# Performance work log

Hardware: AMD Instinct MI355X
Metric: run time of the kernel (lower is better)

The kernel has to match this reference:

```python
import jax, jax.numpy as jnp
import numpy as np

G, B, N, D = 3, 4096, 32, 256
C, H, A, L = 128, 8, 128, 16


def setup_inputs() -> dict:
    key = jax.random.key(0)
    ks = jax.random.split(key, 9)
    return {
        "targets": jax.random.normal(ks[0], (B, D), jnp.float32),
        "contexts": jax.random.normal(ks[1], (G, B, N, D), jnp.float32),
        "kernel": jax.random.normal(ks[2], (D, C), jnp.float32) * 0.05,
        "attn_kernel": jax.random.normal(ks[3], (1, H, 2 * C), jnp.float32) * 0.05,
        "attn_bias": jnp.zeros((H * C,), jnp.float32),
        "sem_kernel": jax.random.normal(ks[4], (H * C, A), jnp.float32) * 0.05,
        "sem_att_kernel": jax.random.normal(ks[5], (A, 1), jnp.float32) * 0.05,
        "dense_w": jax.random.normal(ks[6], (H * C, L), jnp.float32) * 0.05,
        "dense_b": jnp.zeros((L,), jnp.float32),
    }


def reference(targets, contexts, kernel, attn_kernel, attn_bias, sem_kernel,
              sem_att_kernel, dense_w, dense_b):
    # NodeAttention (shared weights across metapath groups; vectorized over G)
    node = jnp.einsum('bd,dc->bc', targets, kernel)            # [B,C]
    neigh = jnp.einsum('gbnd,dc->gbnc', contexts, kernel)      # [G,B,N,C]
    g, b, n, c = neigh.shape
    ak = attn_kernel[0]                                        # [H,2C]
    ak_node, ak_neigh = ak[:, :c], ak[:, c:]                   # split of concat([node, neigh])
    # scores[g,b,n,h] = concat(node_b, neigh_gbn) . ak_h
    scores = (jnp.einsum('bc,hc->bh', node, ak_node)[None, :, None, :]
              + jnp.einsum('gbnc,hc->gbnh', neigh, ak_neigh))  # [G,B,N,H]
    scores = jnp.transpose(scores, (0, 1, 3, 2))               # [G,B,H,N]
    coef = jax.nn.softmax(jax.nn.leaky_relu(scores, 0.2), axis=-1)
    z = jnp.einsum('gbhn,gbnc->gbhc', coef, neigh)             # [G,B,H,C]
    z = z.reshape(g, b, -1) + attn_bias                        # [G,B,H*C] (concat=True)
    # SemanticAttention over metapath groups
    inp = jnp.transpose(z, (1, 0, 2))                          # [B,G,HC]
    s = jnp.squeeze(jnp.matmul(jnp.tanh(jnp.matmul(inp, sem_kernel)), sem_att_kernel), -1)  # [B,G]
    att = jax.nn.softmax(s, axis=-1)
    pooled = jnp.einsum('bg,bgd->bd', att, inp)                # [B,HC]
    logits = pooled @ dense_w + dense_b                        # [B,L]
    return logits
```

## Files before the change

kernel.cpp:

```cpp
#include <hip/hip_runtime.h>

typedef float v4f __attribute__((ext_vector_type(4)));
typedef short v8s __attribute__((ext_vector_type(8)));
typedef short v4s __attribute__((ext_vector_type(4)));

__device__ __forceinline__ unsigned short f2bf(float x){
    unsigned u = __float_as_uint(x);
    u += 0x7FFFu + ((u >> 16) & 1u);
    return (unsigned short)(u >> 16);
}
__device__ __forceinline__ float bf2f(unsigned short h){
    return __uint_as_float(((unsigned)h) << 16);
}

__global__ __launch_bounds__(256) void prep_a(const float* __restrict__ kern,
        const float* __restrict__ ak, float* __restrict__ wn, float* __restrict__ wg){
    int d = threadIdx.x;
    float an[8], ag[8];
    #pragma unroll
    for (int h=0;h<8;h++){ an[h]=0.f; ag[h]=0.f; }
    for (int c=0;c<128;c++){
        float kv = kern[d*128+c];
        #pragma unroll
        for (int h=0;h<8;h++){
            an[h] = fmaf(kv, ak[h*256+c], an[h]);
            ag[h] = fmaf(kv, ak[h*256+128+c], ag[h]);
        }
    }
    #pragma unroll
    for (int h=0;h<8;h++){ wn[d*8+h]=an[h]; wg[d*8+h]=ag[h]; }
}

__global__ __launch_bounds__(256) void prep_b(const float* __restrict__ kern,
        const float* __restrict__ wg, unsigned short* __restrict__ packB){
    int tid = blockIdx.x*256 + threadIdx.x;
    for (int r=0;r<9;r++){
        int e = tid + r*4096;
        int j = e & 7; int rest = e >> 3;
        int l = rest & 63; rest >>= 6;
        int cc = rest % 9; int kk = rest / 9;
        int d = kk*32 + (l>>4)*8 + j;
        int c = cc*16 + (l&15);
        float v;
        if (cc < 8) v = kern[d*128 + c];
        else { int h = c - 128; v = (h < 8) ? wg[d*8+h] : 0.0f; }
        packB[e] = f2bf(v);
    }
}

__global__ __launch_bounds__(256) void prep_c(const float* __restrict__ targ,
        const float* __restrict__ wn, float* __restrict__ ns){
    int b = blockIdx.x*256 + threadIdx.x;
    float acc[8];
    #pragma unroll
    for (int h=0;h<8;h++) acc[h]=0.f;
    for (int d=0; d<256; d++){
        float tv = targ[b*256+d];
        #pragma unroll
        for (int h=0;h<8;h++) acc[h] = fmaf(tv, wn[d*8+h], acc[h]);
    }
    #pragma unroll
    for (int h=0;h<8;h++) ns[b*8+h] = acc[h];
}

__global__ __launch_bounds__(256) void prep_d(const float* __restrict__ semk,
        unsigned short* __restrict__ pack2){
    int tid = blockIdx.x*256 + threadIdx.x;
    for (int r=0;r<16;r++){
        int e = tid + r*8192;
        int j = e & 7; int rest = e >> 3;
        int l = rest & 63; rest >>= 6;
        int cc = rest & 7; rest >>= 3;
        int kk = rest & 7; int kc = rest >> 3;
        int k = kc*256 + kk*32 + (l>>4)*8 + j;
        int a = cc*16 + (l&15);
        pack2[e] = f2bf(semk[k*128 + a]);
    }
}

__global__ __launch_bounds__(256) void phase1(const float* __restrict__ ctx,
        const unsigned short* __restrict__ packB, const float* __restrict__ ns,
        const float* __restrict__ bias, unsigned short* __restrict__ zb16){
    __shared__ __align__(16) unsigned short aT[64*256];
    __shared__ __align__(16) unsigned short outT[64*146];
    __shared__ float cf[2*32*8];

    int t = threadIdx.x;
    int bid = blockIdx.x;
    int g  = bid >> 11;
    int b0 = (bid & 2047) * 2;
    const float* cbase = ctx + (size_t)(g*4096 + b0) * 8192;

    int w = t >> 6, lane = t & 63;
    int ncc = (w==0) ? 3 : 2;
    int ccl[3] = {w, w+4, 8};
    v4f acc[4][3];
    #pragma unroll
    for (int m=0;m<4;m++)
        #pragma unroll
        for (int i=0;i<3;i++) acc[m][i] = (v4f){0.f,0.f,0.f,0.f};

    int srow = t >> 5;
    int sd   = (t & 31) * 4;

    v4f pf[8];
    #pragma unroll
    for (int i=0;i<8;i++)
        pf[i] = *(const v4f*)(cbase + (i*8 + srow)*256 + sd);
    #pragma unroll
    for (int i=0;i<8;i++){
        int row = i*8 + srow;
        v4s h;
        h[0]=(short)f2bf(pf[i][0]); h[1]=(short)f2bf(pf[i][1]);
        h[2]=(short)f2bf(pf[i][2]); h[3]=(short)f2bf(pf[i][3]);
        int byte = row*512 + ((sd*2) ^ ((row&7)<<4));
        *(v4s*)((char*)aT + byte) = h;
    }
    __syncthreads();

    #pragma unroll
    for (int i=0;i<8;i++)
        pf[i] = *(const v4f*)(cbase + (i*8 + srow)*256 + 128 + sd);

    #pragma unroll
    for (int kk=0;kk<4;kk++){
        v8s bfr[3];
        #pragma unroll
        for (int i=0;i<3;i++)
            if (i < ncc)
                bfr[i] = *(const v8s*)(packB + (((kk*9 + ccl[i])*64 + lane) << 3));
        v8s afr[4];
        #pragma unroll
        for (int m=0;m<4;m++){
            int row = m*16 + (lane&15);
            int d0  = kk*32 + (lane>>4)*8;
            int byte = row*512 + ((d0*2) ^ ((row&7)<<4));
            afr[m] = *(const v8s*)((const char*)aT + byte);
        }
        #pragma unroll
        for (int m=0;m<4;m++)
            #pragma unroll
            for (int i=0;i<3;i++)
                if (i < ncc)
                    acc[m][i] = __builtin_amdgcn_mfma_f32_16x16x32_bf16(afr[m], bfr[i], acc[m][i], 0,0,0);
    }

    #pragma unroll
    for (int i=0;i<8;i++){
        int row = i*8 + srow;
        int d = 128 + sd;
        v4s h;
        h[0]=(short)f2bf(pf[i][0]); h[1]=(short)f2bf(pf[i][1]);
        h[2]=(short)f2bf(pf[i][2]); h[3]=(short)f2bf(pf[i][3]);
        int byte = row*512 + ((d*2) ^ ((row&7)<<4));
        *(v4s*)((char*)aT + byte) = h;
    }
    __syncthreads();

    #pragma unroll
    for (int kk=4;kk<8;kk++){
        v8s bfr[3];
        #pragma unroll
        for (int i=0;i<3;i++)
            if (i < ncc)
                bfr[i] = *(const v8s*)(packB + (((kk*9 + ccl[i])*64 + lane) << 3));
        v8s afr[4];
        #pragma unroll
        for (int m=0;m<4;m++){
            int row = m*16 + (lane&15);
            int d0  = kk*32 + (lane>>4)*8;
            int byte = row*512 + ((d0*2) ^ ((row&7)<<4));
            afr[m] = *(const v8s*)((const char*)aT + byte);
        }
        #pragma unroll
        for (int m=0;m<4;m++)
            #pragma unroll
            for (int i=0;i<3;i++)
                if (i < ncc)
                    acc[m][i] = __builtin_amdgcn_mfma_f32_16x16x32_bf16(afr[m], bfr[i], acc[m][i], 0,0,0);
    }

    #pragma unroll
    for (int m=0;m<4;m++)
        #pragma unroll
        for (int i=0;i<3;i++)
            if (i < ncc){
                int col = ccl[i]*16 + (lane&15);
                #pragma unroll
                for (int r=0;r<4;r++){
                    int row = m*16 + (lane>>4)*4 + r;
                    outT[row*146 + col] = f2bf(acc[m][i][r]);
                }
            }
    __syncthreads();

    {
        int p = t >> 4, i = t & 15;
        int b = p >> 3, h = p & 7;
        float nsv = ns[(b0 + b)*8 + h];
        int row0 = b*32 + i, row1 = row0 + 16;
        float s0 = bf2f(outT[row0*146 + 128 + h]) + nsv;
        float s1 = bf2f(outT[row1*146 + 128 + h]) + nsv;
        s0 = s0 > 0.f ? s0 : 0.2f*s0;
        s1 = s1 > 0.f ? s1 : 0.2f*s1;
        float m = fmaxf(s0, s1);
        #pragma unroll
        for (int d=1; d<16; d<<=1) m = fmaxf(m, __shfl_xor(m, d));
        float e0 = __expf(s0 - m), e1 = __expf(s1 - m);
        float ssum = e0 + e1;
        #pragma unroll
        for (int d=1; d<16; d<<=1) ssum += __shfl_xor(ssum, d);
        float inv = 1.0f / ssum;
        cf[(b*32 + i)*8 + h]      = e0 * inv;
        cf[(b*32 + i + 16)*8 + h] = e1 * inv;
    }
    __syncthreads();

    {
        int b = t >> 7, c = t & 127;
        float az[8];
        #pragma unroll
        for (int h=0;h<8;h++) az[h]=0.f;
        for (int n=0;n<32;n++){
            float v = bf2f(outT[(b*32+n)*146 + c]);
            v4f c0 = *(const v4f*)&cf[(b*32+n)*8];
            v4f c1 = *(const v4f*)&cf[(b*32+n)*8 + 4];
            az[0] = fmaf(c0[0], v, az[0]); az[1] = fmaf(c0[1], v, az[1]);
            az[2] = fmaf(c0[2], v, az[2]); az[3] = fmaf(c0[3], v, az[3]);
            az[4] = fmaf(c1[0], v, az[4]); az[5] = fmaf(c1[1], v, az[5]);
            az[6] = fmaf(c1[2], v, az[6]); az[7] = fmaf(c1[3], v, az[7]);
        }
        size_t zb = ((size_t)(b0 + b)*3 + g)*1024;
        #pragma unroll
        for (int h=0;h<8;h++) zb16[zb + h*128 + c] = f2bf(az[h] + bias[h*128 + c]);
    }
}

__global__ __launch_bounds__(256) void semk2(const unsigned short* __restrict__ zb16,
        const unsigned short* __restrict__ pack2, const float* __restrict__ sa,
        float* __restrict__ sws){
    __shared__ float red[16*4];
    int t = threadIdx.x, w = t>>6, lane = t&63;
    int r0 = blockIdx.x * 16;
    v4f acc0 = (v4f){0.f,0.f,0.f,0.f};
    v4f acc1 = (v4f){0.f,0.f,0.f,0.f};
    const unsigned short* abase = zb16 + (size_t)(r0 + (lane&15))*1024 + (lane>>4)*8;
    #pragma unroll 4
    for (int kk=0; kk<32; kk++){
        v8s afr = *(const v8s*)(abase + kk*32);
        v8s b0  = *(const v8s*)(pack2 + (((kk*8 + w  )*64 + lane) << 3));
        v8s b1  = *(const v8s*)(pack2 + (((kk*8 + w+4)*64 + lane) << 3));
        acc0 = __builtin_amdgcn_mfma_f32_16x16x32_bf16(afr, b0, acc0, 0,0,0);
        acc1 = __builtin_amdgcn_mfma_f32_16x16x32_bf16(afr, b1, acc1, 0,0,0);
    }
    float sa0 = sa[w*16 + (lane&15)];
    float sa1 = sa[(w+4)*16 + (lane&15)];
    #pragma unroll
    for (int r=0;r<4;r++){
        float v = fmaf(tanhf(acc0[r]), sa0, tanhf(acc1[r]) * sa1);
        #pragma unroll
        for (int d=1; d<16; d<<=1) v += __shfl_xor(v, d);
        if ((lane&15)==0) red[((lane>>4)*4 + r)*4 + w] = v;
    }
    __syncthreads();
    if (t < 16)
        sws[r0 + t] = red[t*4] + red[t*4+1] + red[t*4+2] + red[t*4+3];
}

__global__ __launch_bounds__(64) void final3(const unsigned short* __restrict__ zb16,
        const float* __restrict__ sws, const float* __restrict__ dw,
        const float* __restrict__ db, float* __restrict__ outp){
    int b = blockIdx.x;
    int lane = threadIdx.x;
    float s0 = sws[b*3], s1 = sws[b*3+1], s2 = sws[b*3+2];
    float m = fmaxf(s0, fmaxf(s1, s2));
    float e0 = __expf(s0-m), e1 = __expf(s1-m), e2 = __expf(s2-m);
    float inv = 1.0f/(e0+e1+e2);
    float a0 = e0*inv, a1 = e1*inv, a2 = e2*inv;

    const unsigned short* z0 = zb16 + (size_t)b*3072 + lane*16;
    v8s za0 = *(const v8s*)(z0);          v8s za1 = *(const v8s*)(z0+8);
    v8s zb0 = *(const v8s*)(z0+1024);     v8s zb1 = *(const v8s*)(z0+1032);
    v8s zc0 = *(const v8s*)(z0+2048);     v8s zc1 = *(const v8s*)(z0+2056);
    float p[16];
    #pragma unroll
    for (int k=0;k<8;k++){
        p[k]   = a0*bf2f((unsigned short)za0[k]) + a1*bf2f((unsigned short)zb0[k]) + a2*bf2f((unsigned short)zc0[k]);
        p[k+8] = a0*bf2f((unsigned short)za1[k]) + a1*bf2f((unsigned short)zb1[k]) + a2*bf2f((unsigned short)zc1[k]);
    }
    float acc[16];
    #pragma unroll
    for (int l=0;l<16;l++) acc[l]=0.f;
    #pragma unroll
    for (int k=0;k<16;k++){
        const float* dr = dw + (lane*16 + k)*16;
        v4f d0 = *(const v4f*)(dr);
        v4f d1 = *(const v4f*)(dr+4);
        v4f d2 = *(const v4f*)(dr+8);
        v4f d3 = *(const v4f*)(dr+12);
        float pk = p[k];
        acc[0]=fmaf(pk,d0[0],acc[0]);  acc[1]=fmaf(pk,d0[1],acc[1]);
        acc[2]=fmaf(pk,d0[2],acc[2]);  acc[3]=fmaf(pk,d0[3],acc[3]);
        acc[4]=fmaf(pk,d1[0],acc[4]);  acc[5]=fmaf(pk,d1[1],acc[5]);
        acc[6]=fmaf(pk,d1[2],acc[6]);  acc[7]=fmaf(pk,d1[3],acc[7]);
        acc[8]=fmaf(pk,d2[0],acc[8]);  acc[9]=fmaf(pk,d2[1],acc[9]);
        acc[10]=fmaf(pk,d2[2],acc[10]); acc[11]=fmaf(pk,d2[3],acc[11]);
        acc[12]=fmaf(pk,d3[0],acc[12]); acc[13]=fmaf(pk,d3[1],acc[13]);
        acc[14]=fmaf(pk,d3[2],acc[14]); acc[15]=fmaf(pk,d3[3],acc[15]);
    }
    #pragma unroll
    for (int l=0;l<16;l++){
        float v = acc[l];
        #pragma unroll
        for (int d=1; d<64; d<<=1) v += __shfl_xor(v, d);
        acc[l] = v;
    }
    float myv = 0.f;
    #pragma unroll
    for (int l=0;l<16;l++) myv = (lane==l) ? acc[l] : myv;
    if (lane < 16) outp[b*16 + lane] = myv + db[lane];
}

extern "C" void kernel_launch(void* const* d_in, const int* in_sizes, int n_in,
                              void* d_out, int out_size, void* d_ws, size_t ws_size,
                              hipStream_t stream) {
    const float* targets  = (const float*)d_in[0];
    const float* contexts = (const float*)d_in[1];
    const float* kern     = (const float*)d_in[2];
    const float* ak       = (const float*)d_in[3];
    const float* bias     = (const float*)d_in[4];
    const float* semk     = (const float*)d_in[5];
    const float* sa       = (const float*)d_in[6];
    const float* dw       = (const float*)d_in[7];
    const float* db       = (const float*)d_in[8];
    float* outp = (float*)d_out;

    char* ws = (char*)d_ws;
    unsigned short* packB = (unsigned short*)(ws);
    float* wn             = (float*)(ws + 73728);
    float* wg             = (float*)(ws + 81920);
    float* nsb            = (float*)(ws + 90112);
    unsigned short* pack2 = (unsigned short*)(ws + 221184);
    unsigned short* zb16  = (unsigned short*)(ws + 483328);
    float* sws            = (float*)(ws + 25649152);

    prep_a<<<1, 256, 0, stream>>>(kern, ak, wn, wg);
    prep_b<<<16, 256, 0, stream>>>(kern, wg, packB);
    prep_c<<<16, 256, 0, stream>>>(targets, wn, nsb);
    prep_d<<<32, 256, 0, stream>>>(semk, pack2);
    phase1<<<6144, 256, 0, stream>>>(contexts, packB, nsb, bias, zb16);
    semk2<<<768, 256, 0, stream>>>(zb16, pack2, sa, sws);
    final3<<<4096, 64, 0, stream>>>(zb16, sws, dw, db, outp);
}
```

Baseline: 227.5 us.

## Fuse prep kernels and load context directly into MFMA fragments without LDS staging

The four preprocessing kernels become one prep_all launch, and each block recomputes the small attention-weight projection in shared memory instead of going through a separate kernel and global buffers. In phase1 each wave now loads its own 16 context rows straight from global memory into bf16 MFMA A-fragments and computes all 9 output column tiles. This drops the 32KB LDS staging buffer and two barriers, and launch bounds now ask for 4 blocks per CU. The cost is more B-fragment loads per wave, less coalesced strided global reads, and a larger accumulator register footprint.

```diff
diff --git a/kernel.cpp b/kernel.cpp
--- a/kernel.cpp
+++ b/kernel.cpp
@@ -1,8 +1,8 @@
 #include <hip/hip_runtime.h>
+#include <hip/hip_bf16.h>
 
 typedef float v4f __attribute__((ext_vector_type(4)));
 typedef short v8s __attribute__((ext_vector_type(8)));
-typedef short v4s __attribute__((ext_vector_type(4)));
 
 __device__ __forceinline__ unsigned short f2bf(float x){
     unsigned u = __float_as_uint(x);
@@ -12,76 +12,91 @@
 __device__ __forceinline__ float bf2f(unsigned short h){
     return __uint_as_float(((unsigned)h) << 16);
 }
-
-__global__ __launch_bounds__(256) void prep_a(const float* __restrict__ kern,
-        const float* __restrict__ ak, float* __restrict__ wn, float* __restrict__ wg){
-    int d = threadIdx.x;
-    float an[8], ag[8];
-    #pragma unroll
-    for (int h=0;h<8;h++){ an[h]=0.f; ag[h]=0.f; }
-    for (int c=0;c<128;c++){
-        float kv = kern[d*128+c];
-        #pragma unroll
-        for (int h=0;h<8;h++){
-            an[h] = fmaf(kv, ak[h*256+c], an[h]);
-            ag[h] = fmaf(kv, ak[h*256+128+c], ag[h]);
-        }
-    }
-    #pragma unroll
-    for (int h=0;h<8;h++){ wn[d*8+h]=an[h]; wg[d*8+h]=ag[h]; }
-}
-
-__global__ __launch_bounds__(256) void prep_b(const float* __restrict__ kern,
-        const float* __restrict__ wg, unsigned short* __restrict__ packB){
-    int tid = blockIdx.x*256 + threadIdx.x;
-    for (int r=0;r<9;r++){
-        int e = tid + r*4096;
-        int j = e & 7; int rest = e >> 3;
-        int l = rest & 63; rest >>= 6;
-        int cc = rest % 9; int kk = rest / 9;
-        int d = kk*32 + (l>>4)*8 + j;
-        int c = cc*16 + (l&15);
-        float v;
-        if (cc < 8) v = kern[d*128 + c];
-        else { int h = c - 128; v = (h < 8) ? wg[d*8+h] : 0.0f; }
-        packB[e] = f2bf(v);
-    }
-}
-
-__global__ __launch_bounds__(256) void prep_c(const float* __restrict__ targ,
-        const float* __restrict__ wn, float* __restrict__ ns){
-    int b = blockIdx.x*256 + threadIdx.x;
-    float acc[8];
-    #pragma unroll
-    for (int h=0;h<8;h++) acc[h]=0.f;
-    for (int d=0; d<256; d++){
-        float tv = targ[b*256+d];
-        #pragma unroll
-        for (int h=0;h<8;h++) acc[h] = fmaf(tv, wn[d*8+h], acc[h]);
-    }
-    #pragma unroll
-    for (int h=0;h<8;h++) ns[b*8+h] = acc[h];
-}
-
-__global__ __launch_bounds__(256) void prep_d(const float* __restrict__ semk,
-        unsigned short* __restrict__ pack2){
-    int tid = blockIdx.x*256 + threadIdx.x;
-    for (int r=0;r<16;r++){
-        int e = tid + r*8192;
-        int j = e & 7; int rest = e >> 3;
-        int l = rest & 63; rest >>= 6;
-        int cc = rest & 7; rest >>= 3;
-        int kk = rest & 7; int kc = rest >> 3;
-        int k = kc*256 + kk*32 + (l>>4)*8 + j;
-        int a = cc*16 + (l&15);
-        pack2[e] = f2bf(semk[k*128 + a]);
-    }
-}
-
-__global__ __launch_bounds__(256) void phase1(const float* __restrict__ ctx,
+__device__ __forceinline__ v8s pack_bf8(v4f a, v4f b){
+    union { v8s s; __hip_bfloat162 h[4]; } u;
+    u.h[0] = __float22bfloat162_rn(float2{a[0],a[1]});
+    u.h[1] = __float22bfloat162_rn(float2{a[2],a[3]});
+    u.h[2] = __float22bfloat162_rn(float2{b[0],b[1]});
+    u.h[3] = __float22bfloat162_rn(float2{b[2],b[3]});
+    return u.s;
+}
+
+__global__ __launch_bounds__(256) void prep_all(const float* __restrict__ targ,
+        const float* __restrict__ kern, const float* __restrict__ ak,
+        const float* __restrict__ semk, float* __restrict__ ns,
+        unsigned short* __restrict__ packB, unsigned short* __restrict__ pack2){
+    __shared__ float wsh[256*8];
+    int blk = blockIdx.x, t = threadIdx.x;
+    if (blk < 16){
+        {
+            float a[8];
+            #pragma unroll
+            for (int h=0;h<8;h++) a[h]=0.f;
+            const float* kr = kern + t*128;
+            for (int c=0;c<128;c++){
+                float kv = kr[c];
+                #pragma unroll
+                for (int h=0;h<8;h++) a[h] = fmaf(kv, ak[h*256+c], a[h]);
+            }
+            #pragma unroll
+            for (int h=0;h<8;h++) wsh[t*8+h]=a[h];
+        }
+        __syncthreads();
+        int b = blk*256 + t;
+        float acc[8];
+        #pragma unroll
+        for (int h=0;h<8;h++) acc[h]=0.f;
+        const float* tr = targ + (size_t)b*256;
+        for (int d=0;d<256;d++){
+            float tv = tr[d];
+            #pragma unroll
+            for (int h=0;h<8;h++) acc[h] = fmaf(tv, wsh[d*8+h], acc[h]);
+        }
+        #pragma unroll
+        for (int h=0;h<8;h++) ns[b*8+h]=acc[h];
+    } else if (blk < 18){
+        {
+            float a[8];
+            #pragma unroll
+            for (int h=0;h<8;h++) a[h]=0.f;
+            const float* kr = kern + t*128;
+            for (int c=0;c<128;c++){
+                float kv = kr[c];
+                #pragma unroll
+                for (int h=0;h<8;h++) a[h] = fmaf(kv, ak[h*256+128+c], a[h]);
+            }
+            #pragma unroll
+            for (int h=0;h<8;h++) wsh[t*8+h]=a[h];
+        }
+        __syncthreads();
+        int gt = (blk-16)*256 + t;
+        for (int r=0;r<72;r++){
+            int e = gt + r*512;
+            int j = e & 7; int l = (e>>3) & 63;
+            int fc = e >> 9; int cc = fc % 9; int kk = fc / 9;
+            int d = kk*32 + (l>>4)*8 + j;
+            int c = cc*16 + (l&15);
+            float v;
+            if (cc < 8) v = kern[d*128 + c];
+            else { int h = c - 128; v = (h < 8) ? wsh[d*8+h] : 0.0f; }
+            packB[e] = f2bf(v);
+        }
+    } else {
+        int gt = (blk-18)*256 + t;
+        for (int r=0;r<16;r++){
+            int e = gt + r*8192;
+            int j = e & 7; int l = (e>>3) & 63;
+            int cc = (e>>9) & 7; int gkk = e >> 12;
+            int k = gkk*32 + (l>>4)*8 + j;
+            int a2 = cc*16 + (l&15);
+            pack2[e] = f2bf(semk[k*128 + a2]);
+        }
+    }
+}
+
+__global__ __launch_bounds__(256,4) void phase1(const float* __restrict__ ctx,
         const unsigned short* __restrict__ packB, const float* __restrict__ ns,
         const float* __restrict__ bias, unsigned short* __restrict__ zb16){
-    __shared__ __align__(16) unsigned short aT[64*256];
     __shared__ __align__(16) unsigned short outT[64*146];
     __shared__ float cf[2*32*8];
 
@@ -89,109 +104,35 @@
     int bid = blockIdx.x;
     int g  = bid >> 11;
     int b0 = (bid & 2047) * 2;
-    const float* cbase = ctx + (size_t)(g*4096 + b0) * 8192;
-
     int w = t >> 6, lane = t & 63;
-    int ncc = (w==0) ? 3 : 2;
-    int ccl[3] = {w, w+4, 8};
-    v4f acc[4][3];
-    #pragma unroll
-    for (int m=0;m<4;m++)
-        #pragma unroll
-        for (int i=0;i<3;i++) acc[m][i] = (v4f){0.f,0.f,0.f,0.f};
-
-    int srow = t >> 5;
-    int sd   = (t & 31) * 4;
-
-    v4f pf[8];
-    #pragma unroll
-    for (int i=0;i<8;i++)
-        pf[i] = *(const v4f*)(cbase + (i*8 + srow)*256 + sd);
-    #pragma unroll
-    for (int i=0;i<8;i++){
-        int row = i*8 + srow;
-        v4s h;
-        h[0]=(short)f2bf(pf[i][0]); h[1]=(short)f2bf(pf[i][1]);
-        h[2]=(short)f2bf(pf[i][2]); h[3]=(short)f2bf(pf[i][3]);
-        int byte = row*512 + ((sd*2) ^ ((row&7)<<4));
-        *(v4s*)((char*)aT + byte) = h;
-    }
-    __syncthreads();
-
-    #pragma unroll
-    for (int i=0;i<8;i++)
-        pf[i] = *(const v4f*)(cbase + (i*8 + srow)*256 + 128 + sd);
-
-    #pragma unroll
-    for (int kk=0;kk<4;kk++){
-        v8s bfr[3];
-        #pragma unroll
-        for (int i=0;i<3;i++)
-            if (i < ncc)
-                bfr[i] = *(const v8s*)(packB + (((kk*9 + ccl[i])*64 + lane) << 3));
-        v8s afr[4];
-        #pragma unroll
-        for (int m=0;m<4;m++){
-            int row = m*16 + (lane&15);
-            int d0  = kk*32 + (lane>>4)*8;
-            int byte = row*512 + ((d0*2) ^ ((row&7)<<4));
-            afr[m] = *(const v8s*)((const char*)aT + byte);
-        }
-        #pragma unroll
-        for (int m=0;m<4;m++)
-            #pragma unroll
-            for (int i=0;i<3;i++)
-                if (i < ncc)
-                    acc[m][i] = __builtin_amdgcn_mfma_f32_16x16x32_bf16(afr[m], bfr[i], acc[m][i], 0,0,0);
-    }
-
-    #pragma unroll
-    for (int i=0;i<8;i++){
-        int row = i*8 + srow;
-        int d = 128 + sd;
-        v4s h;
-        h[0]=(short)f2bf(pf[i][0]); h[1]=(short)f2bf(pf[i][1]);
-        h[2]=(short)f2bf(pf[i][2]); h[3]=(short)f2bf(pf[i][3]);
-        int byte = row*512 + ((d*2) ^ ((row&7)<<4));
-        *(v4s*)((char*)aT + byte) = h;
-    }
-    __syncthreads();
-
-    #pragma unroll
-    for (int kk=4;kk<8;kk++){
-        v8s bfr[3];
-        #pragma unroll
-        for (int i=0;i<3;i++)
-            if (i < ncc)
-                bfr[i] = *(const v8s*)(packB + (((kk*9 + ccl[i])*64 + lane) << 3));
-        v8s afr[4];
-        #pragma unroll
-        for (int m=0;m<4;m++){
-            int row = m*16 + (lane&15);
-            int d0  = kk*32 + (lane>>4)*8;
-            int byte = row*512 + ((d0*2) ^ ((row&7)<<4));
-            afr[m] = *(const v8s*)((const char*)aT + byte);
-        }
-        #pragma unroll
-        for (int m=0;m<4;m++)
-            #pragma unroll
-            for (int i=0;i<3;i++)
-                if (i < ncc)
-                    acc[m][i] = __builtin_amdgcn_mfma_f32_16x16x32_bf16(afr[m], bfr[i], acc[m][i], 0,0,0);
-    }
-
-    #pragma unroll
-    for (int m=0;m<4;m++)
-        #pragma unroll
-        for (int i=0;i<3;i++)
-            if (i < ncc){
-                int col = ccl[i]*16 + (lane&15);
-                #pragma unroll
-                for (int r=0;r<4;r++){
-                    int row = m*16 + (lane>>4)*4 + r;
-                    outT[row*146 + col] = f2bf(acc[m][i][r]);
-                }
-            }
+
+    const float* abase = ctx + (size_t)((g*4096 + b0)*32 + w*16 + (lane&15))*256 + ((lane>>4)*8);
+    const unsigned short* bbase = packB + lane*8;
+
+    v4f acc[9];
+    #pragma unroll
+    for (int i=0;i<9;i++) acc[i] = (v4f){0.f,0.f,0.f,0.f};
+
+    #pragma unroll
+    for (int kk=0;kk<8;kk++){
+        v4f a0 = *(const v4f*)(abase + kk*32);
+        v4f a1 = *(const v4f*)(abase + kk*32 + 4);
+        v8s afr = pack_bf8(a0, a1);
+        #pragma unroll
+        for (int cc=0;cc<9;cc++){
+            v8s bfr = *(const v8s*)(bbase + (kk*9+cc)*512);
+            acc[cc] = __builtin_amdgcn_mfma_f32_16x16x32_bf16(afr, bfr, acc[cc], 0,0,0);
+        }
+    }
+
+    int qr = (lane>>4)*4;
+    #pragma unroll
+    for (int cc=0;cc<9;cc++){
+        int col = cc*16 + (lane&15);
+        #pragma unroll
+        for (int r=0;r<4;r++)
+            outT[(w*16 + qr + r)*146 + col] = f2bf(acc[cc][r]);
+    }
     __syncthreads();
 
     {
@@ -337,17 +278,12 @@
 
     char* ws = (char*)d_ws;
     unsigned short* packB = (unsigned short*)(ws);
-    float* wn             = (float*)(ws + 73728);
-    float* wg             = (float*)(ws + 81920);
-    float* nsb            = (float*)(ws + 90112);
-    unsigned short* pack2 = (unsigned short*)(ws + 221184);
-    unsigned short* zb16  = (unsigned short*)(ws + 483328);
-    float* sws            = (float*)(ws + 25649152);
-
-    prep_a<<<1, 256, 0, stream>>>(kern, ak, wn, wg);
-    prep_b<<<16, 256, 0, stream>>>(kern, wg, packB);
-    prep_c<<<16, 256, 0, stream>>>(targets, wn, nsb);
-    prep_d<<<32, 256, 0, stream>>>(semk, pack2);
+    float* nsb            = (float*)(ws + 73728);
+    unsigned short* pack2 = (unsigned short*)(ws + 204800);
+    unsigned short* zb16  = (unsigned short*)(ws + 466944);
+    float* sws            = (float*)(ws + 25632768);
+
+    prep_all<<<50, 256, 0, stream>>>(targets, kern, ak, semk, nsb, packB, pack2);
     phase1<<<6144, 256, 0, stream>>>(contexts, packB, nsb, bias, zb16);
     semk2<<<768, 256, 0, stream>>>(zb16, pack2, sa, sws);
     final3<<<4096, 64, 0, stream>>>(zb16, sws, dw, db, outp);
```

Result: faster. 218.9 us (-3.8%).
